# Kernel tuning notes

Hardware: AMD Instinct MI355X
Metric: run time of the kernel (lower is better)

Reference implementation:

```python
import jax, jax.numpy as jnp
import numpy as np

K = 20          # knn neighbors (init kwarg k)
LEAK = 0.2      # LeakyReLU negative slope
EPS = 1e-5      # BatchNorm eps


def knn(x, k):
    # x: (B, D, N) -> indices (B, N, K) of k nearest (largest negative sq-dist)
    inner = -2.0 * jnp.einsum('bin,bim->bnm', x, x)
    xx = jnp.sum(x * x, axis=1, keepdims=True)            # (B,1,N)
    pd = -xx - inner - jnp.swapaxes(xx, 1, 2)             # (B,N,N)
    return jax.lax.top_k(pd, k)[1]


def gather_graph_feature(x, idx):
    # x: (B,D,N), idx: (B,N,K) -> (B, 2D, N, K)
    feat = jax.vmap(lambda xb, ib: xb[:, ib])(x, idx)     # (B,D,N,K)
    xc = x[..., None]                                     # (B,D,N,1)
    return jnp.concatenate([feat - xc, jnp.broadcast_to(xc, feat.shape)], axis=1)


def bn_lrelu(y, g, b, axes):
    mu = jnp.mean(y, axis=axes, keepdims=True)
    var = jnp.var(y, axis=axes, keepdims=True)            # biased var (torch BN train)
    shape = [1] * y.ndim
    shape[1] = -1
    y = (y - mu) * jax.lax.rsqrt(var + EPS) * g.reshape(shape) + b.reshape(shape)
    return jnp.where(y >= 0, y, LEAK * y)


def edge_block(x, idx, w, g, b):
    f = gather_graph_feature(x, idx)                      # (B,2D,N,K)
    y = jnp.einsum('oc,bcnk->bonk', w, f)                 # 1x1 Conv2d, no bias
    y = bn_lrelu(y, g, b, (0, 2, 3))
    return jnp.max(y, axis=-1)                            # max over K -> (B,O,N)


def setup_inputs() -> dict:
    key = jax.random.key(0)
    ks = jax.random.split(key, 8)
    B, D, N = 2, 2, 4096
    out_dim = 512
    pts = jax.random.normal(ks[0], (B, D, N), dtype=jnp.float32)
    dims = [(64, 4), (64, 128), (128, 128), (256, 256), (out_dim, 512)]
    inp = {'pts': pts}
    for i, (o, c) in enumerate(dims):
        inp[f'w{i+1}'] = jax.random.normal(ks[i + 1], (o, c), dtype=jnp.float32) * 0.05
        inp[f'g{i+1}'] = jnp.ones((o,), dtype=jnp.float32)
        inp[f'b{i+1}'] = jnp.zeros((o,), dtype=jnp.float32)
    return inp


def reference(pts, w1, g1, b1, w2, g2, b2, w3, g3, b3, w4, g4, b4, w5, g5, b5):
    idx = knn(pts, K)
    x1 = edge_block(pts, idx, w1, g1, b1)   # (B,64,N)
    x2 = edge_block(x1, idx, w2, g2, b2)    # (B,64,N)
    x3 = edge_block(x2, idx, w3, g3, b3)    # (B,128,N)
    x4 = edge_block(x3, idx, w4, g4, b4)    # (B,256,N)
    x = jnp.concatenate([x1, x2, x3, x4], axis=1)         # (B,512,N)
    y = jnp.einsum('oc,bcn->bon', w5, x)                  # 1x1 Conv1d, no bias
    return bn_lrelu(y, g5, b5, (0, 2))
```

## Files before the change

kernel.cpp:

```cpp
#include <hip/hip_runtime.h>
#include <hip/hip_bf16.h>
#include <math.h>

#define BB 2
#define NN 4096
#define PP (BB*NN)
#define KK 20
#define LEAK 0.2f
#define EPSB 1e-5f

typedef short sv8 __attribute__((ext_vector_type(8)));
typedef float f4  __attribute__((ext_vector_type(4)));

__device__ inline unsigned short f2bf(float f) {
    unsigned u = __float_as_uint(f);
    unsigned r = (u + 0x7FFFu + ((u >> 16) & 1u)) >> 16;
    return (unsigned short)r;
}
__device__ inline float bf2f(unsigned short h) {
    return __uint_as_float((unsigned)h << 16);
}
__device__ inline void gload16(const void* g, void* l) {
    __builtin_amdgcn_global_load_lds(
        (const __attribute__((address_space(1))) unsigned int*)g,
        (__attribute__((address_space(3))) unsigned int*)l, 16, 0, 0);
}

__global__ __launch_bounds__(256) void knn_kernel(const float* __restrict__ pts,
                                                  int* __restrict__ idx,
                                                  const float* __restrict__ w1,
                                                  float* __restrict__ u1,
                                                  float* __restrict__ v1) {
    __shared__ unsigned int hist[256];
    __shared__ unsigned int scanres[3];
    __shared__ unsigned int cnt2[2];
    __shared__ unsigned long long blist[512];

    int r = blockIdx.x;
    int b = r >> 12, n = r & (NN - 1);
    const float* X0 = pts + (size_t)b * 2 * NN;
    const float* X1 = X0 + NN;
    int tid = threadIdx.x;
    float x0n = X0[n], x1n = X1[n];
    float xxn = __fadd_rn(__fmul_rn(x0n, x0n), __fmul_rn(x1n, x1n));
    float negxxn = __fsub_rn(0.f, xxn);

    if (tid < 64) {
        float4 wr = *(const float4*)&w1[(size_t)tid * 4];
        u1[(size_t)r * 64 + tid] = fmaf(wr.x, x0n, wr.y * x1n);
        v1[(size_t)r * 64 + tid] = fmaf(wr.z - wr.x, x0n, (wr.w - wr.y) * x1n);
    }

    float pdv[16];
    #pragma unroll
    for (int q = 0; q < 16; ++q) {
        int m = q * 256 + tid;
        float x0m = X0[m], x1m = X1[m];
        float xxm = __fadd_rn(__fmul_rn(x0m, x0m), __fmul_rn(x1m, x1m));
        float dot = __builtin_fmaf(x1n, x1m, __fmul_rn(x0n, x0m));
        float inner = __fmul_rn(-2.f, dot);
        float t1 = __fsub_rn(negxxn, inner);
        pdv[q] = __fsub_rn(t1, xxm);
    }

    int bins[16];
    int shift = 24;
    for (int attempt = 0; attempt < 3; ++attempt) {
        hist[tid] = 0;
        __syncthreads();
        float scale = (float)(1u << shift);
        #pragma unroll
        for (int q = 0; q < 16; ++q) {
            float s = fmaxf(-pdv[q], 0.f);
            unsigned int ki = (unsigned int)fminf(s * scale, 4.294e9f);
            unsigned int bin = ki >> 16;
            if (bin > 255u) bin = 255u;
            bins[q] = (int)bin;
            if (bin < 255u) atomicAdd(&hist[bin], 1u);
        }
        __syncthreads();
        if (tid < 64) {
            uint4 hv = *(const uint4*)&hist[tid * 4];
            unsigned int p0 = hv.x, p1 = p0 + hv.y, p2 = p1 + hv.z, p3 = p2 + hv.w;
            unsigned int lanesum = p3, inc = p3;
            #pragma unroll
            for (int s2 = 1; s2 < 64; s2 <<= 1) {
                unsigned int o = __shfl_up(inc, s2, 64);
                if (tid >= s2) inc += o;
            }
            unsigned int excl = inc - lanesum;
            bool flag = (inc >= KK);
            unsigned long long bal = __ballot(flag);
            int firstlane = (bal == 0ULL) ? -1 : (__ffsll((long long)bal) - 1);
            if (tid == 0) scanres[0] = (bal != 0ULL) ? 1u : 0u;
            if (tid == firstlane) {
                unsigned int c0 = excl + p0, c1 = excl + p1, c2 = excl + p2;
                int t = (c0 >= KK) ? 0 : (c1 >= KK) ? 1 : (c2 >= KK) ? 2 : 3;
                unsigned int cumb = (t == 0) ? excl : (t == 1) ? c0 : (t == 2) ? c1 : c2;
                scanres[1] = (unsigned)(tid * 4 + t);
                scanres[2] = cumb;
            }
        }
        __syncthreads();
        if (scanres[0]) break;
        shift -= 6;
        __syncthreads();
    }

    int bstar = (int)scanres[1];
    unsigned int cumb = scanres[2];
    if (tid == 0) { cnt2[0] = 0; cnt2[1] = 0; }
    __syncthreads();

    #pragma unroll
    for (int q = 0; q < 16; ++q) {
        int bin = bins[q];
        int m = q * 256 + tid;
        if (bin < bstar) {
            unsigned int slot = atomicAdd(&cnt2[0], 1u);
            idx[(size_t)r * KK + slot] = m;
        } else if (bin == bstar) {
            unsigned int pos = atomicAdd(&cnt2[1], 1u);
            if (pos < 512u) {
                unsigned int ub = __float_as_uint(pdv[q]);
                unsigned int fk = (ub & 0x80000000u) ? ~ub : (ub | 0x80000000u);
                blist[pos] = ((unsigned long long)(~fk) << 32) | (unsigned int)m;
            }
        }
    }
    __syncthreads();

    int need = KK - (int)cumb;
    int L = (int)min(cnt2[1], 512u);
    if (tid < 64) {
        unsigned long long e[8];
        #pragma unroll
        for (int i = 0; i < 8; ++i) {
            int p = tid + 64 * i;
            e[i] = (p < L) ? blist[p] : ~0ULL;
        }
        unsigned long long lmin = e[0];
        #pragma unroll
        for (int i = 1; i < 8; ++i) lmin = (e[i] < lmin) ? e[i] : lmin;
        for (int p = 0; p < need; ++p) {
            unsigned long long gm = lmin;
            #pragma unroll
            for (int s2 = 32; s2 > 0; s2 >>= 1) {
                unsigned long long o = __shfl_xor(gm, s2, 64);
                if (o < gm) gm = o;
            }
            if (lmin == gm) {
                #pragma unroll
                for (int i = 0; i < 8; ++i) if (e[i] == gm) e[i] = ~0ULL;
                lmin = e[0];
                #pragma unroll
                for (int i = 1; i < 8; ++i) lmin = (e[i] < lmin) ? e[i] : lmin;
                idx[(size_t)r * KK + cumb + p] = (int)(gm & 0xFFFFFFFFu);
            }
        }
    }
}

__global__ __launch_bounds__(256) void convert_all(const float* __restrict__ w2,
                                                   const float* __restrict__ w3,
                                                   const float* __restrict__ w4,
                                                   const float* __restrict__ w5,
                                                   unsigned short* __restrict__ bh,
                                                   unsigned short* __restrict__ bl) {
    int i = blockIdx.x * 256 + threadIdx.x;
    if (i >= 352256) return;
    const float* w; int O, C, mode, base;
    if (i < 8192)       { w = w2; O = 64;  C = 64;  mode = 0; base = 0; }
    else if (i < 24576) { w = w3; O = 128; C = 64;  mode = 0; base = 8192; }
    else if (i < 90112) { w = w4; O = 256; C = 128; mode = 0; base = 24576; }
    else                { w = w5; O = 512; C = 512; mode = 1; base = 90112; }
    int j = i - base;
    int row = j / C, c = j - row * C;
    float v;
    if (mode == 0) {
        if (row < O) v = w[(size_t)row * 2 * C + c];
        else {
            const float* wr = w + (size_t)(row - O) * 2 * C;
            v = wr[C + c] - wr[c];
        }
    } else {
        v = w[(size_t)row * C + c];
    }
    unsigned short h = f2bf(v);
    bh[i] = h;
    bl[i] = f2bf(v - bf2f(h));
}

__global__ __launch_bounds__(256) void mfma_gemm64(const unsigned short* __restrict__ Xh,
                                                   const unsigned short* __restrict__ Xl,
                                                   int ldx, int K,
                                                   const unsigned short* __restrict__ Bh,
                                                   const unsigned short* __restrict__ Bl,
                                                   int O,
                                                   float* __restrict__ outU,
                                                   float* __restrict__ outV) {
    __shared__ unsigned short Ah[256 * 8], Al[256 * 8], Bhs[256 * 8], Bls[256 * 8];
    int row0 = blockIdx.x * 64, col0 = blockIdx.y * 64;
    int tid = threadIdx.x;
    int wid = tid >> 6, lane = tid & 63;
    int wm = wid & 1, wn = wid >> 1;
    int l15 = lane & 15, l4 = lane >> 4;
    int m = tid & 63, kb = tid >> 6;

    f4 acc[2][2];
    #pragma unroll
    for (int i = 0; i < 2; ++i)
        #pragma unroll
        for (int j = 0; j < 2; ++j) { acc[i][j][0]=0.f; acc[i][j][1]=0.f; acc[i][j][2]=0.f; acc[i][j][3]=0.f; }

    for (int k0 = 0; k0 < K; k0 += 32) {
        size_t ga = (size_t)(row0 + m) * ldx + k0 + kb * 8;
        size_t gb = (size_t)(col0 + m) * K + k0 + kb * 8;
        gload16(Xh + ga, &Ah[(size_t)(wid * 64) * 8]);
        gload16(Xl + ga, &Al[(size_t)(wid * 64) * 8]);
        gload16(Bh + gb, &Bhs[(size_t)(wid * 64) * 8]);
        gload16(Bl + gb, &Bls[(size_t)(wid * 64) * 8]);
        __syncthreads();

        sv8 bhf[2], blf[2];
        #pragma unroll
        for (int fn = 0; fn < 2; ++fn) {
            int nn2 = wn * 32 + fn * 16 + l15;
            bhf[fn] = *(const sv8*)&Bhs[(size_t)(l4 * 64 + nn2) * 8];
            blf[fn] = *(const sv8*)&Bls[(size_t)(l4 * 64 + nn2) * 8];
        }
        #pragma unroll
        for (int fm = 0; fm < 2; ++fm) {
            int mm = wm * 32 + fm * 16 + l15;
            sv8 ah = *(const sv8*)&Ah[(size_t)(l4 * 64 + mm) * 8];
            sv8 al = *(const sv8*)&Al[(size_t)(l4 * 64 + mm) * 8];
            #pragma unroll
            for (int fn = 0; fn < 2; ++fn) {
                acc[fm][fn] = __builtin_amdgcn_mfma_f32_16x16x32_bf16(ah, bhf[fn], acc[fm][fn], 0, 0, 0);
                acc[fm][fn] = __builtin_amdgcn_mfma_f32_16x16x32_bf16(ah, blf[fn], acc[fm][fn], 0, 0, 0);
                acc[fm][fn] = __builtin_amdgcn_mfma_f32_16x16x32_bf16(al, bhf[fn], acc[fm][fn], 0, 0, 0);
            }
        }
        __syncthreads();
    }

    #pragma unroll
    for (int fm = 0; fm < 2; ++fm) {
        int rbase = row0 + wm * 32 + fm * 16 + l4 * 4;
        #pragma unroll
        for (int fn = 0; fn < 2; ++fn) {
            int jg = col0 + wn * 32 + fn * 16 + l15;
            #pragma unroll
            for (int e = 0; e < 4; ++e) {
                float vv = acc[fm][fn][e];
                int p = rbase + e;
                if (jg < O) outU[(size_t)p * O + jg] = vv;
                else        outV[(size_t)p * O + (jg - O)] = vv;
            }
        }
    }
}

__global__ __launch_bounds__(256) void mfma_gemm128s(const unsigned short* __restrict__ Xh,
                                                     int ldx, int K,
                                                     const unsigned short* __restrict__ Bh,
                                                     int O,
                                                     float* __restrict__ outU,
                                                     float* __restrict__ partial) {
    __shared__ unsigned short Ah[512 * 8], Bhs[512 * 8];
    __shared__ float sred1[2][128], sred2[2][128];
    int row0 = blockIdx.x * 128, col0 = blockIdx.y * 128;
    int tid = threadIdx.x;
    int wid = tid >> 6, lane = tid & 63;
    int wm = wid & 1, wn = wid >> 1;
    int l15 = lane & 15, l4 = lane >> 4;

    f4 acc[4][4];
    #pragma unroll
    for (int i = 0; i < 4; ++i)
        #pragma unroll
        for (int j = 0; j < 4; ++j) { acc[i][j][0]=0.f; acc[i][j][1]=0.f; acc[i][j][2]=0.f; acc[i][j][3]=0.f; }

    for (int k0 = 0; k0 < K; k0 += 32) {
        #pragma unroll
        for (int j = 0; j < 2; ++j) {
            int c = tid + 256 * j;
            int m = c & 127, kb = c >> 7;
            size_t ga = (size_t)(row0 + m) * ldx + k0 + kb * 8;
            size_t gb = (size_t)(col0 + m) * K + k0 + kb * 8;
            gload16(Xh + ga, &Ah[(size_t)(wid * 64 + 256 * j) * 8]);
            gload16(Bh + gb, &Bhs[(size_t)(wid * 64 + 256 * j) * 8]);
        }
        __syncthreads();

        sv8 bhf[4];
        #pragma unroll
        for (int fn = 0; fn < 4; ++fn) {
            int nn2 = wn * 64 + fn * 16 + l15;
            bhf[fn] = *(const sv8*)&Bhs[(size_t)(l4 * 128 + nn2) * 8];
        }
        #pragma unroll
        for (int fm = 0; fm < 4; ++fm) {
            int mm = wm * 64 + fm * 16 + l15;
            sv8 ah = *(const sv8*)&Ah[(size_t)(l4 * 128 + mm) * 8];
            #pragma unroll
            for (int fn = 0; fn < 4; ++fn)
                acc[fm][fn] = __builtin_amdgcn_mfma_f32_16x16x32_bf16(ah, bhf[fn], acc[fm][fn], 0, 0, 0);
        }
        __syncthreads();
    }

    #pragma unroll
    for (int fm = 0; fm < 4; ++fm) {
        int rbase = row0 + wm * 64 + fm * 16 + l4 * 4;
        #pragma unroll
        for (int fn = 0; fn < 4; ++fn) {
            int jg = col0 + wn * 64 + fn * 16 + l15;
            #pragma unroll
            for (int e = 0; e < 4; ++e)
                outU[(size_t)(rbase + e) * O + jg] = acc[fm][fn][e];
        }
    }

    #pragma unroll
    for (int fn = 0; fn < 4; ++fn) {
        float a1 = 0.f, a2 = 0.f;
        #pragma unroll
        for (int fm = 0; fm < 4; ++fm)
            #pragma unroll
            for (int e = 0; e < 4; ++e) { float t = acc[fm][fn][e]; a1 += t; a2 = fmaf(t, t, a2); }
        a1 += __shfl_xor(a1, 16, 64); a2 += __shfl_xor(a2, 16, 64);
        a1 += __shfl_xor(a1, 32, 64); a2 += __shfl_xor(a2, 32, 64);
        if (lane < 16) {
            int cb = wn * 64 + fn * 16 + lane;
            sred1[wm][cb] = a1;
            sred2[wm][cb] = a2;
        }
    }
    __syncthreads();
    if (tid < 128) {
        float s1 = sred1[0][tid] + sred1[1][tid];
        float s2 = sred2[0][tid] + sred2[1][tid];
        size_t pbase = (size_t)blockIdx.x * 1024 + (size_t)(col0 + tid) * 2;
        partial[pbase]     = s1;
        partial[pbase + 1] = s2;
    }
}

__global__ __launch_bounds__(256) void edge_stats(const float* __restrict__ u,
                                                  const float* __restrict__ v,
                                                  const int* __restrict__ idx,
                                                  int O, int PPL,
                                                  float* __restrict__ mx, float* __restrict__ mn,
                                                  float* __restrict__ partial) {
    __shared__ float red[4 * 256];
    int tid = threadIdx.x;
    int CH2 = O >> 1;
    int PS = 256 / CH2;
    int co = tid % CH2;
    int ps = tid / CH2;
    float s1a = 0.f, s1b = 0.f, s2a = 0.f, s2b = 0.f;
    for (int pi = 0; pi < PPL; ++pi) {
        int r = (blockIdx.x * PS + ps) * PPL + pi;
        int b = r >> 12;
        const float* ub = u + (size_t)b * NN * O + 2 * co;
        float2 vv = *(const float2*)&v[(size_t)r * O + 2 * co];
        const int* ip = idx + (size_t)r * KK;
        int mreg[KK];
        #pragma unroll
        for (int k = 0; k < KK; ++k) mreg[k] = ip[k];
        float2 uv[KK];
        #pragma unroll
        for (int k = 0; k < KK; ++k) uv[k] = *(const float2*)&ub[(size_t)mreg[k] * O];
        float bxa = -INFINITY, bxb = -INFINITY, bna = INFINITY, bnb = INFINITY;
        #pragma unroll
        for (int k = 0; k < KK; ++k) {
            float y0 = uv[k].x + vv.x, y1 = uv[k].y + vv.y;
            s1a += y0; s2a = fmaf(y0, y0, s2a);
            s1b += y1; s2b = fmaf(y1, y1, s2b);
            bxa = fmaxf(bxa, y0); bna = fminf(bna, y0);
            bxb = fmaxf(bxb, y1); bnb = fminf(bnb, y1);
        }
        *(float2*)&mx[(size_t)r * O + 2 * co] = make_float2(bxa, bxb);
        *(float2*)&mn[(size_t)r * O + 2 * co] = make_float2(bna, bnb);
    }
    red[0 * 256 + tid] = s1a;
    red[1 * 256 + tid] = s1b;
    red[2 * 256 + tid] = s2a;
    red[3 * 256 + tid] = s2b;
    __syncthreads();
    for (int s = PS >> 1; s > 0; s >>= 1) {
        if (ps < s) {
            int oth = tid + s * CH2;
            red[0 * 256 + tid] += red[0 * 256 + oth];
            red[1 * 256 + tid] += red[1 * 256 + oth];
            red[2 * 256 + tid] += red[2 * 256 + oth];
            red[3 * 256 + tid] += red[3 * 256 + oth];
        }
        __syncthreads();
    }
    if (ps == 0) {
        size_t base = (size_t)blockIdx.x * 2 * O;
        partial[base + 2 * co]         = red[0 * 256 + tid];
        partial[base + 2 * co + 1]     = red[1 * 256 + tid];
        partial[base + O + 2 * co]     = red[2 * 256 + tid];
        partial[base + O + 2 * co + 1] = red[3 * 256 + tid];
    }
}

__global__ __launch_bounds__(256) void stats_reduce(const float* __restrict__ partial, int nblk,
                                                    int O, float cnt,
                                                    const float* __restrict__ g,
                                                    const float* __restrict__ bsh,
                                                    float* __restrict__ st) {
    __shared__ float r1[4], r2[4];
    int o = blockIdx.x, tid = threadIdx.x;
    float s1 = 0.f, s2 = 0.f;
    for (int bk = tid; bk < nblk; bk += 256) {
        size_t base = (size_t)bk * 2 * O;
        s1 += partial[base + o];
        s2 += partial[base + O + o];
    }
    #pragma unroll
    for (int s = 32; s > 0; s >>= 1) {
        s1 += __shfl_down(s1, s, 64);
        s2 += __shfl_down(s2, s, 64);
    }
    if ((tid & 63) == 0) { r1[tid >> 6] = s1; r2[tid >> 6] = s2; }
    __syncthreads();
    if (tid == 0) {
        s1 = r1[0] + r1[1] + r1[2] + r1[3];
        s2 = r2[0] + r2[1] + r2[2] + r2[3];
        float mu = s1 / cnt;
        float var = s2 / cnt - mu * mu;
        float x = var + EPSB;
        float rr = rsqrtf(x);
        rr = rr * (1.5f - 0.5f * x * rr * rr);
        float sc = g[o] * rr;
        st[o] = sc;
        st[O + o] = bsh[o] - mu * sc;
    }
}

__global__ void apply_edge(const float* __restrict__ mx, const float* __restrict__ mn,
                           const float* __restrict__ st, int O, int choff,
                           unsigned short* __restrict__ xh, unsigned short* __restrict__ xl,
                           int writelo) {
    int e2 = blockIdx.x * 256 + threadIdx.x;
    int half = O >> 1;
    if (e2 >= PP * half) return;
    int r = e2 / half, o = (e2 - r * half) * 2;
    float2 sc = *(const float2*)&st[o];
    float2 tt = *(const float2*)&st[O + o];
    float2 vx = *(const float2*)&mx[(size_t)r * O + o];
    float2 vn = *(const float2*)&mn[(size_t)r * O + o];
    float b0 = (sc.x >= 0.f) ? vx.x : vn.x;
    float b1 = (sc.y >= 0.f) ? vx.y : vn.y;
    float y0 = fmaf(sc.x, b0, tt.x); y0 = (y0 >= 0.f) ? y0 : LEAK * y0;
    float y1 = fmaf(sc.y, b1, tt.y); y1 = (y1 >= 0.f) ? y1 : LEAK * y1;
    unsigned short h0 = f2bf(y0), h1 = f2bf(y1);
    size_t d = (size_t)r * 512 + choff + o;
    ((unsigned int*)xh)[d >> 1] = (unsigned int)h0 | ((unsigned int)h1 << 16);
    if (writelo) {
        unsigned short l0 = f2bf(y0 - bf2f(h0)), l1 = f2bf(y1 - bf2f(h1));
        ((unsigned int*)xl)[d >> 1] = (unsigned int)l0 | ((unsigned int)l1 << 16);
    }
}

__global__ __launch_bounds__(64) void final_reduce(const float* __restrict__ partial,
                                                   float cnt,
                                                   const float* __restrict__ g,
                                                   const float* __restrict__ bsh,
                                                   float* __restrict__ st) {
    int c = blockIdx.x, tid = threadIdx.x;
    size_t base = (size_t)tid * 1024 + (size_t)c * 2;
    float s1 = partial[base], s2 = partial[base + 1];
    #pragma unroll
    for (int s = 32; s > 0; s >>= 1) {
        s1 += __shfl_down(s1, s, 64);
        s2 += __shfl_down(s2, s, 64);
    }
    if (tid == 0) {
        float mu = s1 / cnt;
        float var = s2 / cnt - mu * mu;
        float x = var + EPSB;
        float rr = rsqrtf(x);
        rr = rr * (1.5f - 0.5f * x * rr * rr);
        float sc = g[c] * rr;
        st[c] = sc;
        st[512 + c] = bsh[c] - mu * sc;
    }
}

__global__ __launch_bounds__(256) void final_apply(const float* __restrict__ y5,
                                                   const float* __restrict__ st,
                                                   float* __restrict__ out) {
    __shared__ float tile[32][33];
    int n0 = blockIdx.x * 32, o0 = blockIdx.y * 32, b = blockIdx.z;
    int tx = threadIdx.x, ty = threadIdx.y;
    for (int i = 0; i < 4; ++i) {
        int nl = ty + i * 8;
        tile[nl][tx] = y5[((size_t)(b * NN + n0 + nl)) * 512 + o0 + tx];
    }
    __syncthreads();
    for (int i = 0; i < 4; ++i) {
        int ol = ty + i * 8;
        int o = o0 + ol;
        float sc = st[o], tt = st[512 + o];
        float yv = fmaf(sc, tile[tx][ol], tt);
        yv = (yv >= 0.f) ? yv : LEAK * yv;
        out[((size_t)b * 512 + o) * NN + n0 + tx] = yv;
    }
}

extern "C" void kernel_launch(void* const* d_in, const int* in_sizes, int n_in,
                              void* d_out, int out_size, void* d_ws, size_t ws_size,
                              hipStream_t stream) {
    const float* pts = (const float*)d_in[0];
    const float* w[5]; const float* g[5]; const float* bsh[5];
    for (int i = 0; i < 5; ++i) {
        w[i]   = (const float*)d_in[1 + 3 * i];
        g[i]   = (const float*)d_in[2 + 3 * i];
        bsh[i] = (const float*)d_in[3 + 3 * i];
    }
    float* out = (float*)d_out;

    unsigned short* xh = (unsigned short*)d_ws;
    unsigned short* xl = xh + (size_t)PP * 512;
    float* u    = (float*)(xl + (size_t)PP * 512);
    float* v    = u    + (size_t)PP * 256;
    float* mxb  = v    + (size_t)PP * 256;
    float* mnb  = mxb  + (size_t)PP * 256;
    float* y5   = mxb;
    int*   idxb = (int*)(mnb + (size_t)PP * 256);
    float* part = (float*)(idxb + (size_t)PP * KK);
    float* st   = part + (size_t)1048576;
    unsigned short* wh_all = (unsigned short*)(st + 1024);
    unsigned short* wl_all = wh_all + 352256;

    knn_kernel<<<PP, 256, 0, stream>>>(pts, idxb, w[0], u, v);
    convert_all<<<1376, 256, 0, stream>>>(w[1], w[2], w[3], w[4], wh_all, wl_all);

    const int Cs[4]    = {2, 64, 64, 128};
    const int Os[4]    = {64, 64, 128, 256};
    const int choffs[4]= {0, 64, 128, 256};
    const int inoffs[4]= {0, 0, 64, 128};
    const int woffs[4] = {0, 0, 8192, 24576};

    for (int li = 0; li < 4; ++li) {
        int C = Cs[li], O = Os[li];
        if (li > 0) {
            dim3 gg(PP / 64, (2 * O) / 64);
            mfma_gemm64<<<gg, 256, 0, stream>>>(xh + inoffs[li], xl + inoffs[li], 512, C,
                                                wh_all + woffs[li], wl_all + woffs[li], O, u, v);
        }
        int PS  = 512 / O;
        int PPL = (O == 256) ? 2 : 1;
        int nblk = PP / (PS * PPL);
        edge_stats<<<nblk, 256, 0, stream>>>(u, v, idxb, O, PPL, mxb, mnb, part);
        stats_reduce<<<O, 256, 0, stream>>>(part, nblk, O, (float)((size_t)PP * KK),
                                            g[li], bsh[li], st);
        apply_edge<<<(PP * O / 2 + 255) / 256, 256, 0, stream>>>(
            mxb, mnb, st, O, choffs[li], xh, xl, (li == 3) ? 0 : 1);
    }

    dim3 gf(PP / 128, 512 / 128);
    mfma_gemm128s<<<gf, 256, 0, stream>>>(xh, 512, 512, wh_all + 90112, 512, y5, part);
    final_reduce<<<512, 64, 0, stream>>>(part, (float)PP, g[4], bsh[4], st);
    final_apply<<<dim3(NN / 32, 512 / 32, BB), dim3(32, 8), 0, stream>>>(y5, st, out);
}
```

Measured before the change: 188.5 us.

## Replace partial-sum BN reductions with atomics and fold stats into apply kernels

Folds the weight bf16 conversion and the zeroing of the accumulators into the knn kernel, so their separate launches go away. BatchNorm sums are now accumulated with atomicAdd into a small global buffer instead of per-block partials, and the mean/variance finalisation is recomputed inside the apply kernels. This removes six launches (stats_reduce per layer, final_reduce, convert_all) and their serialisation points. In exchange it adds atomic contention, order-dependent float summation, and redundant rsqrt work in every apply thread.

```diff
diff --git a/kernel.cpp b/kernel.cpp
--- a/kernel.cpp
+++ b/kernel.cpp
@@ -30,17 +30,53 @@
                                                   int* __restrict__ idx,
                                                   const float* __restrict__ w1,
                                                   float* __restrict__ u1,
-                                                  float* __restrict__ v1) {
+                                                  float* __restrict__ v1,
+                                                  const float* __restrict__ w2,
+                                                  const float* __restrict__ w3,
+                                                  const float* __restrict__ w4,
+                                                  const float* __restrict__ w5,
+                                                  unsigned short* __restrict__ wh_all,
+                                                  unsigned short* __restrict__ wl_all,
+                                                  float* __restrict__ acc_all) {
     __shared__ unsigned int hist[256];
     __shared__ unsigned int scanres[3];
     __shared__ unsigned int cnt2[2];
     __shared__ unsigned long long blist[512];
 
     int r = blockIdx.x;
+    int tid = threadIdx.x;
+
+    if (r < 1376) {
+        int i = r * 256 + tid;
+        if (i < 352256) {
+            const float* w; int O, C, mode, base;
+            if (i < 8192)       { w = w2; O = 64;  C = 64;  mode = 0; base = 0; }
+            else if (i < 24576) { w = w3; O = 128; C = 64;  mode = 0; base = 8192; }
+            else if (i < 90112) { w = w4; O = 256; C = 128; mode = 0; base = 24576; }
+            else                { w = w5; O = 512; C = 512; mode = 1; base = 90112; }
+            int j = i - base;
+            int row = j / C, c = j - row * C;
+            float v;
+            if (mode == 0) {
+                if (row < O) v = w[(size_t)row * 2 * C + c];
+                else {
+                    const float* wr = w + (size_t)(row - O) * 2 * C;
+                    v = wr[C + c] - wr[c];
+                }
+            } else {
+                v = w[(size_t)row * C + c];
+            }
+            unsigned short h = f2bf(v);
+            wh_all[i] = h;
+            wl_all[i] = f2bf(v - bf2f(h));
+        }
+    } else if (r >= 4096 && r < 4108) {
+        acc_all[(r - 4096) * 256 + tid] = 0.f;
+    }
+
     int b = r >> 12, n = r & (NN - 1);
     const float* X0 = pts + (size_t)b * 2 * NN;
     const float* X1 = X0 + NN;
-    int tid = threadIdx.x;
     float x0n = X0[n], x1n = X1[n];
     float xxn = __fadd_rn(__fmul_rn(x0n, x0n), __fmul_rn(x1n, x1n));
     float negxxn = __fsub_rn(0.f, xxn);
@@ -159,36 +195,6 @@
             }
         }
     }
-}
-
-__global__ __launch_bounds__(256) void convert_all(const float* __restrict__ w2,
-                                                   const float* __restrict__ w3,
-                                                   const float* __restrict__ w4,
-                                                   const float* __restrict__ w5,
-                                                   unsigned short* __restrict__ bh,
-                                                   unsigned short* __restrict__ bl) {
-    int i = blockIdx.x * 256 + threadIdx.x;
-    if (i >= 352256) return;
-    const float* w; int O, C, mode, base;
-    if (i < 8192)       { w = w2; O = 64;  C = 64;  mode = 0; base = 0; }
-    else if (i < 24576) { w = w3; O = 128; C = 64;  mode = 0; base = 8192; }
-    else if (i < 90112) { w = w4; O = 256; C = 128; mode = 0; base = 24576; }
-    else                { w = w5; O = 512; C = 512; mode = 1; base = 90112; }
-    int j = i - base;
-    int row = j / C, c = j - row * C;
-    float v;
-    if (mode == 0) {
-        if (row < O) v = w[(size_t)row * 2 * C + c];
-        else {
-            const float* wr = w + (size_t)(row - O) * 2 * C;
-            v = wr[C + c] - wr[c];
-        }
-    } else {
-        v = w[(size_t)row * C + c];
-    }
-    unsigned short h = f2bf(v);
-    bh[i] = h;
-    bl[i] = f2bf(v - bf2f(h));
 }
 
 __global__ __launch_bounds__(256) void mfma_gemm64(const unsigned short* __restrict__ Xh,
@@ -266,7 +272,7 @@
                                                      const unsigned short* __restrict__ Bh,
                                                      int O,
                                                      float* __restrict__ outU,
-                                                     float* __restrict__ partial) {
+                                                     float* __restrict__ facc) {
     __shared__ unsigned short Ah[512 * 8], Bhs[512 * 8];
     __shared__ float sred1[2][128], sred2[2][128];
     int row0 = blockIdx.x * 128, col0 = blockIdx.y * 128;
@@ -341,9 +347,8 @@
     if (tid < 128) {
         float s1 = sred1[0][tid] + sred1[1][tid];
         float s2 = sred2[0][tid] + sred2[1][tid];
-        size_t pbase = (size_t)blockIdx.x * 1024 + (size_t)(col0 + tid) * 2;
-        partial[pbase]     = s1;
-        partial[pbase + 1] = s2;
+        atomicAdd(&facc[(size_t)(col0 + tid) * 2],     s1);
+        atomicAdd(&facc[(size_t)(col0 + tid) * 2 + 1], s2);
     }
 }
 
@@ -352,7 +357,7 @@
                                                   const int* __restrict__ idx,
                                                   int O, int PPL,
                                                   float* __restrict__ mx, float* __restrict__ mn,
-                                                  float* __restrict__ partial) {
+                                                  float* __restrict__ accL) {
     __shared__ float red[4 * 256];
     int tid = threadIdx.x;
     int CH2 = O >> 1;
@@ -400,64 +405,41 @@
         __syncthreads();
     }
     if (ps == 0) {
-        size_t base = (size_t)blockIdx.x * 2 * O;
-        partial[base + 2 * co]         = red[0 * 256 + tid];
-        partial[base + 2 * co + 1]     = red[1 * 256 + tid];
-        partial[base + O + 2 * co]     = red[2 * 256 + tid];
-        partial[base + O + 2 * co + 1] = red[3 * 256 + tid];
-    }
-}
-
-__global__ __launch_bounds__(256) void stats_reduce(const float* __restrict__ partial, int nblk,
-                                                    int O, float cnt,
-                                                    const float* __restrict__ g,
-                                                    const float* __restrict__ bsh,
-                                                    float* __restrict__ st) {
-    __shared__ float r1[4], r2[4];
-    int o = blockIdx.x, tid = threadIdx.x;
-    float s1 = 0.f, s2 = 0.f;
-    for (int bk = tid; bk < nblk; bk += 256) {
-        size_t base = (size_t)bk * 2 * O;
-        s1 += partial[base + o];
-        s2 += partial[base + O + o];
-    }
-    #pragma unroll
-    for (int s = 32; s > 0; s >>= 1) {
-        s1 += __shfl_down(s1, s, 64);
-        s2 += __shfl_down(s2, s, 64);
-    }
-    if ((tid & 63) == 0) { r1[tid >> 6] = s1; r2[tid >> 6] = s2; }
-    __syncthreads();
-    if (tid == 0) {
-        s1 = r1[0] + r1[1] + r1[2] + r1[3];
-        s2 = r2[0] + r2[1] + r2[2] + r2[3];
-        float mu = s1 / cnt;
-        float var = s2 / cnt - mu * mu;
-        float x = var + EPSB;
-        float rr = rsqrtf(x);
-        rr = rr * (1.5f - 0.5f * x * rr * rr);
-        float sc = g[o] * rr;
-        st[o] = sc;
-        st[O + o] = bsh[o] - mu * sc;
+        atomicAdd(&accL[4 * co + 0], red[0 * 256 + tid]);
+        atomicAdd(&accL[4 * co + 1], red[2 * 256 + tid]);
+        atomicAdd(&accL[4 * co + 2], red[1 * 256 + tid]);
+        atomicAdd(&accL[4 * co + 3], red[3 * 256 + tid]);
     }
 }
 
 __global__ void apply_edge(const float* __restrict__ mx, const float* __restrict__ mn,
-                           const float* __restrict__ st, int O, int choff,
+                           const float* __restrict__ accL,
+                           const float* __restrict__ g, const float* __restrict__ bsh,
+                           int O, int choff, float cnt,
                            unsigned short* __restrict__ xh, unsigned short* __restrict__ xl,
                            int writelo) {
     int e2 = blockIdx.x * 256 + threadIdx.x;
     int half = O >> 1;
     if (e2 >= PP * half) return;
-    int r = e2 / half, o = (e2 - r * half) * 2;
-    float2 sc = *(const float2*)&st[o];
-    float2 tt = *(const float2*)&st[O + o];
+    int r = e2 / half, co = e2 - r * half;
+    int o = 2 * co;
+    float4 a = *(const float4*)&accL[4 * co];
+    float mu0 = a.x / cnt, mu1 = a.z / cnt;
+    float var0 = a.y / cnt - mu0 * mu0;
+    float var1 = a.w / cnt - mu1 * mu1;
+    float x0 = var0 + EPSB, x1 = var1 + EPSB;
+    float r0 = rsqrtf(x0); r0 = r0 * (1.5f - 0.5f * x0 * r0 * r0);
+    float r1 = rsqrtf(x1); r1 = r1 * (1.5f - 0.5f * x1 * r1 * r1);
+    float2 gg = *(const float2*)&g[o];
+    float2 bb = *(const float2*)&bsh[o];
+    float sc0 = gg.x * r0, sc1 = gg.y * r1;
+    float tt0 = bb.x - mu0 * sc0, tt1 = bb.y - mu1 * sc1;
     float2 vx = *(const float2*)&mx[(size_t)r * O + o];
     float2 vn = *(const float2*)&mn[(size_t)r * O + o];
-    float b0 = (sc.x >= 0.f) ? vx.x : vn.x;
-    float b1 = (sc.y >= 0.f) ? vx.y : vn.y;
-    float y0 = fmaf(sc.x, b0, tt.x); y0 = (y0 >= 0.f) ? y0 : LEAK * y0;
-    float y1 = fmaf(sc.y, b1, tt.y); y1 = (y1 >= 0.f) ? y1 : LEAK * y1;
+    float b0 = (sc0 >= 0.f) ? vx.x : vn.x;
+    float b1 = (sc1 >= 0.f) ? vx.y : vn.y;
+    float y0 = fmaf(sc0, b0, tt0); y0 = (y0 >= 0.f) ? y0 : LEAK * y0;
+    float y1 = fmaf(sc1, b1, tt1); y1 = (y1 >= 0.f) ? y1 : LEAK * y1;
     unsigned short h0 = f2bf(y0), h1 = f2bf(y1);
     size_t d = (size_t)r * 512 + choff + o;
     ((unsigned int*)xh)[d >> 1] = (unsigned int)h0 | ((unsigned int)h1 << 16);
@@ -467,33 +449,11 @@
     }
 }
 
-__global__ __launch_bounds__(64) void final_reduce(const float* __restrict__ partial,
-                                                   float cnt,
+__global__ __launch_bounds__(256) void final_apply(const float* __restrict__ y5,
+                                                   const float* __restrict__ facc,
                                                    const float* __restrict__ g,
                                                    const float* __restrict__ bsh,
-                                                   float* __restrict__ st) {
-    int c = blockIdx.x, tid = threadIdx.x;
-    size_t base = (size_t)tid * 1024 + (size_t)c * 2;
-    float s1 = partial[base], s2 = partial[base + 1];
-    #pragma unroll
-    for (int s = 32; s > 0; s >>= 1) {
-        s1 += __shfl_down(s1, s, 64);
-        s2 += __shfl_down(s2, s, 64);
-    }
-    if (tid == 0) {
-        float mu = s1 / cnt;
-        float var = s2 / cnt - mu * mu;
-        float x = var + EPSB;
-        float rr = rsqrtf(x);
-        rr = rr * (1.5f - 0.5f * x * rr * rr);
-        float sc = g[c] * rr;
-        st[c] = sc;
-        st[512 + c] = bsh[c] - mu * sc;
-    }
-}
-
-__global__ __launch_bounds__(256) void final_apply(const float* __restrict__ y5,
-                                                   const float* __restrict__ st,
+                                                   float cnt,
                                                    float* __restrict__ out) {
     __shared__ float tile[32][33];
     int n0 = blockIdx.x * 32, o0 = blockIdx.y * 32, b = blockIdx.z;
@@ -506,7 +466,14 @@
     for (int i = 0; i < 4; ++i) {
         int ol = ty + i * 8;
         int o = o0 + ol;
-        float sc = st[o], tt = st[512 + o];
+        float2 a = *(const float2*)&facc[(size_t)o * 2];
+        float mu = a.x / cnt;
+        float var = a.y / cnt - mu * mu;
+        float x = var + EPSB;
+        float rr = rsqrtf(x);
+        rr = rr * (1.5f - 0.5f * x * rr * rr);
+        float sc = g[o] * rr;
+        float tt = bsh[o] - mu * sc;
         float yv = fmaf(sc, tile[tx][ol], tt);
         yv = (yv >= 0.f) ? yv : LEAK * yv;
         out[((size_t)b * 512 + o) * NN + n0 + tx] = yv;
@@ -533,19 +500,20 @@
     float* mnb  = mxb  + (size_t)PP * 256;
     float* y5   = mxb;
     int*   idxb = (int*)(mnb + (size_t)PP * 256);
-    float* part = (float*)(idxb + (size_t)PP * KK);
-    float* st   = part + (size_t)1048576;
-    unsigned short* wh_all = (unsigned short*)(st + 1024);
+    float* acc_all = (float*)(idxb + (size_t)PP * KK);
+    unsigned short* wh_all = (unsigned short*)(acc_all + 3072);
     unsigned short* wl_all = wh_all + 352256;
 
-    knn_kernel<<<PP, 256, 0, stream>>>(pts, idxb, w[0], u, v);
-    convert_all<<<1376, 256, 0, stream>>>(w[1], w[2], w[3], w[4], wh_all, wl_all);
-
-    const int Cs[4]    = {2, 64, 64, 128};
-    const int Os[4]    = {64, 64, 128, 256};
-    const int choffs[4]= {0, 64, 128, 256};
-    const int inoffs[4]= {0, 0, 64, 128};
-    const int woffs[4] = {0, 0, 8192, 24576};
+    knn_kernel<<<PP, 256, 0, stream>>>(pts, idxb, w[0], u, v,
+                                       w[1], w[2], w[3], w[4], wh_all, wl_all, acc_all);
+
+    const int Cs[4]     = {2, 64, 64, 128};
+    const int Os[4]     = {64, 64, 128, 256};
+    const int choffs[4] = {0, 64, 128, 256};
+    const int inoffs[4] = {0, 0, 64, 128};
+    const int woffs[4]  = {0, 0, 8192, 24576};
+    const int aoffs[4]  = {0, 512, 1024, 1536};
+    float cntE = (float)((size_t)PP * KK);
 
     for (int li = 0; li < 4; ++li) {
         int C = Cs[li], O = Os[li];
@@ -557,15 +525,14 @@
         int PS  = 512 / O;
         int PPL = (O == 256) ? 2 : 1;
         int nblk = PP / (PS * PPL);
-        edge_stats<<<nblk, 256, 0, stream>>>(u, v, idxb, O, PPL, mxb, mnb, part);
-        stats_reduce<<<O, 256, 0, stream>>>(part, nblk, O, (float)((size_t)PP * KK),
-                                            g[li], bsh[li], st);
+        edge_stats<<<nblk, 256, 0, stream>>>(u, v, idxb, O, PPL, mxb, mnb, acc_all + aoffs[li]);
         apply_edge<<<(PP * O / 2 + 255) / 256, 256, 0, stream>>>(
-            mxb, mnb, st, O, choffs[li], xh, xl, (li == 3) ? 0 : 1);
+            mxb, mnb, acc_all + aoffs[li], g[li], bsh[li], O, choffs[li], cntE,
+            xh, xl, (li == 3) ? 0 : 1);
     }
 
     dim3 gf(PP / 128, 512 / 128);
-    mfma_gemm128s<<<gf, 256, 0, stream>>>(xh, 512, 512, wh_all + 90112, 512, y5, part);
-    final_reduce<<<512, 64, 0, stream>>>(part, (float)PP, g[4], bsh[4], st);
-    final_apply<<<dim3(NN / 32, 512 / 32, BB), dim3(32, 8), 0, stream>>>(y5, st, out);
-}
+    mfma_gemm128s<<<gf, 256, 0, stream>>>(xh, 512, 512, wh_all + 90112, 512, y5, acc_all + 2048);
+    final_apply<<<dim3(NN / 32, 512 / 32, BB), dim3(32, 8), 0, stream>>>(
+        y5, acc_all + 2048, g[4], bsh[4], (float)PP, out);
+}
```

After: 734.9 us. 290% more time.
